# Performance work log

Hardware: AMD Instinct MI355X
Metric: run time of the kernel (lower is better)

Reference implementation:

```python
import jax, jax.numpy as jnp
import numpy as np

ROPE_BASE = 10000.0
WINDOW = 1024  # per_layer_sliding_window
SCALE = 0.08838834764831845  # 1/sqrt(128)
NEG_INF = -1e30


def _apply_rope(x, positions):
    # x: [B, S, H, D]; positions: [B, S] int
    D = x.shape[-1]
    inv_freq = 1.0 / (ROPE_BASE ** (jnp.arange(0, D, 2, dtype=jnp.float32) / D))  # [D/2]
    ang = positions.astype(jnp.float32)[..., None] * inv_freq          # [B, S, D/2]
    cos = jnp.cos(ang)[:, :, None, :]                                   # [B, S, 1, D/2]
    sin = jnp.sin(ang)[:, :, None, :]
    x1, x2 = x[..., : D // 2], x[..., D // 2 :]
    return jnp.concatenate([x1 * cos - x2 * sin, x2 * cos + x1 * sin], axis=-1)


def setup_inputs() -> dict:
    key = jax.random.key(0)
    k1, k2, k3, k4 = jax.random.split(key, 4)
    B, S, H, KV, D = 1, 2048, 32, 8, 128
    q = jax.random.normal(k1, (B, S, H, D), dtype=jnp.float32)
    k = jax.random.normal(k2, (B, S, KV, D), dtype=jnp.float32)
    v = jax.random.normal(k3, (B, S, KV, D), dtype=jnp.float32)
    positions = jnp.broadcast_to(jnp.arange(S, dtype=jnp.int32), (B, S))
    sinks = jax.random.normal(k4, (H,), dtype=jnp.float32)
    return {"q": q, "k": k, "v": v, "positions": positions, "sinks": sinks}


def reference(q, k, v, positions, sinks):
    # q: [B,S,H,D]; k,v: [B,S,KV,D]; positions: [B,S]; sinks: [H]
    B, S, H, D = q.shape
    KV = k.shape[2]
    group = H // KV

    qr = _apply_rope(q, positions)
    kr = _apply_rope(k, positions)

    # GQA: expand kv heads to match q heads
    kr = jnp.repeat(kr, group, axis=2)  # [B,S,H,D]
    ve = jnp.repeat(v, group, axis=2)   # [B,S,H,D]

    scores = jnp.einsum("bqhd,bkhd->bhqk", qr, kr) * SCALE  # [B,H,Q,K]

    pq = positions[:, :, None]  # [B,Q,1]
    pk = positions[:, None, :]  # [B,1,K]
    allowed = (pk <= pq) & (pq - pk < WINDOW)               # causal + sliding window
    scores = jnp.where(allowed[:, None, :, :], scores, NEG_INF)

    # softmax with per-head attention sink logit in the denominator
    sink = sinks[None, :, None]                             # [1,H,1]
    m = jnp.maximum(jnp.max(scores, axis=-1), sink)         # [B,H,Q]
    p = jnp.exp(scores - m[..., None])                      # [B,H,Q,K]
    denom = jnp.sum(p, axis=-1) + jnp.exp(sink - m)         # [B,H,Q]
    out = jnp.einsum("bhqk,bkhd->bqhd", p, ve) / denom.transpose(0, 2, 1)[..., None]
    return out  # [B,S,H,D]
```

## Files before the change

kernel.cpp:

```cpp
#include <hip/hip_runtime.h>

#define S_LEN 2048
#define NH 32
#define NKV 8
#define HD 128
#define WINDOW 1024
#define SCALEF 0.08838834764831845f
#define NEG_INF_F -1e30f
#define NEG_L2_10K_O64 -0.2076205059304601f
#define LOG2E 1.442695040888963f
#define CSHIFT_L2 17.31234049067355f

typedef unsigned short ushort_t;
typedef __attribute__((ext_vector_type(8))) short short8;
typedef __attribute__((ext_vector_type(4))) float floatx4;
typedef __attribute__((ext_vector_type(4))) int intx4;

static __device__ __forceinline__ float fexp2(float x) {
  return __builtin_amdgcn_exp2f(x);
}

static __device__ __forceinline__ ushort_t f2bf(float f) {
  union { float f; unsigned u; } un; un.f = f;
  unsigned r = un.u + 0x7fffu + ((un.u >> 16) & 1u);
  return (ushort_t)(r >> 16);
}

static __device__ __forceinline__ unsigned pack2bf(float a, float b) {
  return (unsigned)f2bf(a) | ((unsigned)f2bf(b) << 16);
}

__device__ __forceinline__ void gl_lds16(const ushort_t* g, ushort_t* l) {
  __builtin_amdgcn_global_load_lds(
      (const __attribute__((address_space(1))) unsigned int*)g,
      (__attribute__((address_space(3))) unsigned int*)l, 16, 0, 0);
}

__global__ __launch_bounds__(256) void prep_kv(
    const float* __restrict__ k, const float* __restrict__ v,
    const int* __restrict__ positions, ushort_t* __restrict__ Kr,
    ushort_t* __restrict__ Vt) {
  __shared__ float lv[64][129];
  const int kv = blockIdx.x & 7;
  const int s0 = (blockIdx.x >> 3) * 64;
  const int tid = threadIdx.x;

  {
    const int i = tid & 63;
    const int wrow = tid >> 6;
    const float invf = fexp2((float)i * NEG_L2_10K_O64);
#pragma unroll 4
    for (int it = 0; it < 16; ++it) {
      int s = s0 + it * 4 + wrow;
      float pos = (float)positions[s];
      const float* kp = k + ((size_t)s * NKV + kv) * HD;
      float x1 = kp[i], x2 = kp[i + 64];
      float sn, cs;
      __sincosf(pos * invf, &sn, &cs);
      ushort_t* o = Kr + ((size_t)kv * S_LEN + s) * HD;
      o[i] = f2bf(x1 * cs - x2 * sn);
      o[i + 64] = f2bf(x2 * cs + x1 * sn);
    }
  }
  {
    const int d = tid & 127;
    const int r2 = tid >> 7;
#pragma unroll
    for (int it = 0; it < 32; ++it) {
      int row = it * 2 + r2;
      lv[row][d] = v[((size_t)(s0 + row) * NKV + kv) * HD + d];
    }
  }
  __syncthreads();
  {
    const int ss = tid & 63;
    const int d0 = tid >> 6;
#pragma unroll
    for (int it = 0; it < 32; ++it) {
      int d = d0 + it * 4;
      Vt[((size_t)kv * HD + d) * S_LEN + s0 + ss] = f2bf(lv[ss][d]);
    }
  }
}

__global__ __launch_bounds__(256, 4) void attn_kernel(
    const float* __restrict__ q, const int* __restrict__ positions,
    const float* __restrict__ sinks, const ushort_t* __restrict__ Kr,
    const ushort_t* __restrict__ Vt, float* __restrict__ out) {
  __shared__ __align__(16) ushort_t smem[16384];

  const int tid = threadIdx.x;
  const int w = tid >> 6;
  const int lane = tid & 63;
  const int quad = lane >> 4;
  const int l16 = lane & 15;
  const int kv = blockIdx.x & 7;
  const int tile = blockIdx.x >> 3;
  const int h = kv * 4 + w;
  const int q0 = tile * 16;

  ushort_t* Qsw = smem + w * 2048;
  {
    const float invf = fexp2((float)lane * NEG_L2_10K_O64);
#pragma unroll 4
    for (int row = 0; row < 16; ++row) {
      float pos = (float)positions[q0 + row];
      const float* qp = q + ((size_t)(q0 + row) * NH + h) * HD;
      float x1 = qp[lane], x2 = qp[lane + 64];
      float sn, cs;
      __sincosf(pos * invf, &sn, &cs);
      float o1 = (x1 * cs - x2 * sn) * SCALEF;
      float o2 = (x2 * cs + x1 * sn) * SCALEF;
      int c1_ = (lane >> 3) ^ row;
      int c2_ = ((lane >> 3) + 8) ^ row;
      Qsw[row * 128 + c1_ * 8 + (lane & 7)] = f2bf(o1);
      Qsw[row * 128 + c2_ * 8 + (lane & 7)] = f2bf(o2);
    }
  }
  short8 qf[4];
#pragma unroll
  for (int t = 0; t < 4; ++t)
    qf[t] = *(const short8*)&Qsw[l16 * 128 + (((4 * t + quad) ^ l16) * 8)];
  __syncthreads();

  const ushort_t* KrH = Kr + (size_t)kv * S_LEN * HD;
  const ushort_t* VtH = Vt + (size_t)kv * HD * S_LEN;
  int kgo[2], vgo[2], ldst[2];
#pragma unroll
  for (int i = 0; i < 2; ++i) {
    int slot = i * 256 + tid;
    int key = slot >> 4;
    int cin = (slot & 15) ^ (key & 15);
    kgo[i] = key * HD + cin * 8;
    int d = slot >> 2;
    int qcin = (slot & 3) ^ ((d ^ (d >> 2)) & 3);
    vgo[i] = d * S_LEN + qcin * 8;
    ldst[i] = (i * 256 + (tid & 192)) * 8;
  }

  auto stage = [&](int b, int koff) {
#pragma unroll
    for (int i = 0; i < 2; ++i) {
      gl_lds16(KrH + (size_t)koff * HD + kgo[i], smem + b * 4096 + ldst[i]);
      gl_lds16(VtH + koff + vgo[i], smem + 8192 + b * 4096 + ldst[i]);
    }
  };

  floatx4 O4[8];
#pragma unroll
  for (int i = 0; i < 8; ++i) O4[i] = (floatx4){0.f, 0.f, 0.f, 0.f};
  float lsum = 0.f;

  const int cbeg = (q0 > 1023) ? ((q0 - 1023) >> 5) : 0;
  const int cend = (q0 + 15) >> 5;

  stage(0, cbeg * 32);
  __syncthreads();

  for (int ci = cbeg; ci <= cend; ++ci) {
    const int b = (ci - cbeg) & 1;
    const int koff = ci * 32;
    if (ci < cend) stage(b ^ 1, koff + 32);

    const ushort_t* KsB = smem + b * 4096;
    const ushort_t* VsB = smem + 8192 + b * 4096;

    floatx4 s0v = (floatx4){0.f, 0.f, 0.f, 0.f};
    floatx4 s1v = (floatx4){0.f, 0.f, 0.f, 0.f};
#pragma unroll
    for (int t = 0; t < 4; ++t) {
      int ch = ((4 * t + quad) ^ l16) * 8;
      short8 k0 = *(const short8*)&KsB[l16 * 128 + ch];
      short8 k1 = *(const short8*)&KsB[(l16 + 16) * 128 + ch];
      s0v = __builtin_amdgcn_mfma_f32_16x16x32_bf16(k0, qf[t], s0v, 0, 0, 0);
      s1v = __builtin_amdgcn_mfma_f32_16x16x32_bf16(k1, qf[t], s1v, 0, 0, 0);
    }

    if (koff + 31 > q0 || koff < q0 - 1008) {
      const int qp_ = q0 + l16;
#pragma unroll
      for (int r = 0; r < 4; ++r) {
        int k0i = koff + quad * 4 + r, k1i = k0i + 16;
        if (!((k0i <= qp_) && (qp_ - k0i < WINDOW))) s0v[r] = NEG_INF_F;
        if (!((k1i <= qp_) && (qp_ - k1i < WINDOW))) s1v[r] = NEG_INF_F;
      }
    }

    float pc0[4], pc1[4];
#pragma unroll
    for (int r = 0; r < 4; ++r) {
      pc0[r] = fexp2(fmaf(s0v[r], LOG2E, -CSHIFT_L2));
      pc1[r] = fexp2(fmaf(s1v[r], LOG2E, -CSHIFT_L2));
    }
    lsum += (pc0[0] + pc0[1]) + (pc0[2] + pc0[3]) +
            (pc1[0] + pc1[1]) + (pc1[2] + pc1[3]);

    unsigned pk0[2] = {pack2bf(pc0[0], pc0[1]), pack2bf(pc0[2], pc0[3])};
    unsigned pk1[2] = {pack2bf(pc1[0], pc1[1]), pack2bf(pc1[2], pc1[3])};
    intx4 bi;
    const int sbase = ((quad & 1) * 2) * 16 + l16;
#pragma unroll
    for (int u = 0; u < 4; ++u) {
      int src = sbase + (u >> 1) * 16;
      int lo = __shfl((int)pk0[u & 1], src);
      int hi = __shfl((int)pk1[u & 1], src);
      bi[u] = (quad < 2) ? lo : hi;
    }
    short8 pb = __builtin_bit_cast(short8, bi);

#pragma unroll
    for (int i = 0; i < 8; ++i) {
      int d = 16 * i + l16;
      short8 vf = *(const short8*)&VsB[d * 32 + ((quad ^ ((d ^ (d >> 2)) & 3)) * 8)];
      O4[i] = __builtin_amdgcn_mfma_f32_16x16x32_bf16(vf, pb, O4[i], 0, 0, 0);
    }

    __syncthreads();
  }

  lsum += __shfl_xor(lsum, 16);
  lsum += __shfl_xor(lsum, 32);
  lsum += fexp2(fmaf(sinks[h], LOG2E, -CSHIFT_L2));
  const float rl = 1.0f / lsum;

  float* op = out + ((size_t)(q0 + l16) * NH + h) * HD;
#pragma unroll
  for (int i = 0; i < 8; ++i) {
    floatx4 val = O4[i] * rl;
    *(floatx4*)(op + 16 * i + quad * 4) = val;
  }
}

extern "C" void kernel_launch(void* const* d_in, const int* in_sizes, int n_in,
                              void* d_out, int out_size, void* d_ws, size_t ws_size,
                              hipStream_t stream) {
  const float* q = (const float*)d_in[0];
  const float* k = (const float*)d_in[1];
  const float* v = (const float*)d_in[2];
  const int* positions = (const int*)d_in[3];
  const float* sinks = (const float*)d_in[4];
  float* out = (float*)d_out;

  ushort_t* Kr = (ushort_t*)d_ws;
  ushort_t* Vt = Kr + (size_t)NKV * S_LEN * HD;

  prep_kv<<<NKV * (S_LEN / 64), 256, 0, stream>>>(k, v, positions, Kr, Vt);
  attn_kernel<<<NKV * (S_LEN / 16), 256, 0, stream>>>(q, positions, sinks, Kr, Vt, out);
}
```

Before: 148.5 us.

## Restructure attention with 32x32 MFMA, key-split warps, paired tiles, and blocked V layout

Each warp now covers two query heads and half of each 32-key chunk, and uses 32x32x16 MFMAs for the PV product. Partial outputs from the two key halves are reduced through LDS at the end. Query tiles are paired (a short tile with a long one) so that 768 blocks carry balanced causal/window work. V is stored in 64-key blocked tiles, the softmax scale is folded into Q, and bf16 packing of probabilities uses a cheaper truncate-with-round-add plus perm. This adds LDS reduction traffic, more syncs, and fewer blocks with launch bounds lowered to 3.

```diff
diff --git a/kernel.cpp b/kernel.cpp
--- a/kernel.cpp
+++ b/kernel.cpp
@@ -5,15 +5,14 @@
 #define NKV 8
 #define HD 128
 #define WINDOW 1024
-#define SCALEF 0.08838834764831845f
 #define NEG_INF_F -1e30f
 #define NEG_L2_10K_O64 -0.2076205059304601f
-#define LOG2E 1.442695040888963f
-#define CSHIFT_L2 17.31234049067355f
+#define LOG2E_F 1.442695040888963f
 
 typedef unsigned short ushort_t;
 typedef __attribute__((ext_vector_type(8))) short short8;
 typedef __attribute__((ext_vector_type(4))) float floatx4;
+typedef __attribute__((ext_vector_type(16))) float floatx16;
 typedef __attribute__((ext_vector_type(4))) int intx4;
 
 static __device__ __forceinline__ float fexp2(float x) {
@@ -28,6 +27,12 @@
 
 static __device__ __forceinline__ unsigned pack2bf(float a, float b) {
   return (unsigned)f2bf(a) | ((unsigned)f2bf(b) << 16);
+}
+
+static __device__ __forceinline__ unsigned packP(float a, float b) {
+  unsigned ua = __builtin_bit_cast(unsigned, a) + 0x8000u;
+  unsigned ub = __builtin_bit_cast(unsigned, b) + 0x8000u;
+  return __builtin_amdgcn_perm(ub, ua, 0x07060302u);
 }
 
 __device__ __forceinline__ void gl_lds16(const ushort_t* g, ushort_t* l) {
@@ -44,7 +49,6 @@
   const int kv = blockIdx.x & 7;
   const int s0 = (blockIdx.x >> 3) * 64;
   const int tid = threadIdx.x;
-
   {
     const int i = tid & 63;
     const int wrow = tid >> 6;
@@ -73,161 +77,230 @@
   }
   __syncthreads();
   {
-    const int ss = tid & 63;
-    const int d0 = tid >> 6;
-#pragma unroll
-    for (int it = 0; it < 32; ++it) {
-      int d = d0 + it * 4;
-      Vt[((size_t)kv * HD + d) * S_LEN + s0 + ss] = f2bf(lv[ss][d]);
+    unsigned* Vreg = (unsigned*)(Vt + ((size_t)(kv * 32 + (s0 >> 6)) * HD) * 64);
+#pragma unroll
+    for (int it = 0; it < 16; ++it) {
+      int idx = it * 256 + tid;
+      int d = idx >> 5, j = idx & 31;
+      Vreg[idx] = pack2bf(lv[2 * j][d], lv[2 * j + 1][d]);
     }
   }
 }
 
-__global__ __launch_bounds__(256, 4) void attn_kernel(
+__global__ __launch_bounds__(256, 3) void attn_kernel(
     const float* __restrict__ q, const int* __restrict__ positions,
     const float* __restrict__ sinks, const ushort_t* __restrict__ Kr,
     const ushort_t* __restrict__ Vt, float* __restrict__ out) {
   __shared__ __align__(16) ushort_t smem[16384];
+  __shared__ float lsx[64];
 
   const int tid = threadIdx.x;
   const int w = tid >> 6;
   const int lane = tid & 63;
   const int quad = lane >> 4;
   const int l16 = lane & 15;
+  const int hp = w >> 1;
+  const int kh = w & 1;
   const int kv = blockIdx.x & 7;
-  const int tile = blockIdx.x >> 3;
-  const int h = kv * 4 + w;
-  const int q0 = tile * 16;
-
-  ushort_t* Qsw = smem + w * 2048;
-  {
-    const float invf = fexp2((float)lane * NEG_L2_10K_O64);
+  const int bid = blockIdx.x >> 3;
+  const int h0 = kv * 4 + hp * 2;
+  const float QSCALE = (float)(0.08838834764831845 * 1.4426950408889634);
+
+  const ushort_t* KrH = Kr + (size_t)kv * S_LEN * HD;
+  const ushort_t* VtH = Vt + (size_t)kv * 32 * HD * 64;
+
+  int tiles[2];
+  int ntiles;
+  if (bid < 64) { tiles[0] = bid + 64; tiles[1] = 0; ntiles = 1; }
+  else          { tiles[0] = bid - 64; tiles[1] = 127 - bid; ntiles = 2; }
+
+  int kgo0, kgo1, vgo0, vgo1;
+  { int key = tid >> 4;          kgo0 = key * HD + (((tid & 15) ^ (key & 15)) * 8); }
+  { int s2 = 256 + tid; int key = s2 >> 4;
+                                 kgo1 = key * HD + (((s2 & 15) ^ (key & 15)) * 8); }
+  { int d = tid >> 2;            vgo0 = d * 64 + (((tid & 3) ^ (d & 3)) * 8); }
+  { int d = 64 + (tid >> 2);     vgo1 = d * 64 + (((tid & 3) ^ (d & 3)) * 8); }
+  const int kdst0 = (tid & 192) * 8;
+  const int kdst1 = (256 + (tid & 192)) * 8;
+  const int vdst0 = 8192 + (tid & 192) * 8;
+  const int vdst1 = 8192 + 2048 + (tid & 192) * 8;
+  const int vroff = ((2 * kh + (lane >> 5)) ^ (lane & 3)) * 8;
+
+  auto stage = [&](int b, int koff) {
+    const ushort_t* kb = KrH + (size_t)koff * HD;
+    const ushort_t* vb = VtH + (size_t)(koff >> 6) * HD * 64 + (koff & 32);
+    gl_lds16(kb + kgo0, smem + b * 4096 + kdst0);
+    gl_lds16(kb + kgo1, smem + b * 4096 + kdst1);
+    gl_lds16(vb + vgo0, smem + b * 4096 + vdst0);
+    gl_lds16(vb + vgo1, smem + b * 4096 + vdst1);
+  };
+
+  for (int ti = 0; ti < ntiles; ++ti) {
+    const int tile = tiles[ti];
+    const int q0 = tile * 16;
+
+    {
+      const int hw = kv * 4 + w;
+      ushort_t* Qsw = smem + w * 2048;
+      const float invf = fexp2((float)lane * NEG_L2_10K_O64);
 #pragma unroll 4
-    for (int row = 0; row < 16; ++row) {
-      float pos = (float)positions[q0 + row];
-      const float* qp = q + ((size_t)(q0 + row) * NH + h) * HD;
-      float x1 = qp[lane], x2 = qp[lane + 64];
-      float sn, cs;
-      __sincosf(pos * invf, &sn, &cs);
-      float o1 = (x1 * cs - x2 * sn) * SCALEF;
-      float o2 = (x2 * cs + x1 * sn) * SCALEF;
-      int c1_ = (lane >> 3) ^ row;
-      int c2_ = ((lane >> 3) + 8) ^ row;
-      Qsw[row * 128 + c1_ * 8 + (lane & 7)] = f2bf(o1);
-      Qsw[row * 128 + c2_ * 8 + (lane & 7)] = f2bf(o2);
-    }
-  }
-  short8 qf[4];
-#pragma unroll
-  for (int t = 0; t < 4; ++t)
-    qf[t] = *(const short8*)&Qsw[l16 * 128 + (((4 * t + quad) ^ l16) * 8)];
-  __syncthreads();
-
-  const ushort_t* KrH = Kr + (size_t)kv * S_LEN * HD;
-  const ushort_t* VtH = Vt + (size_t)kv * HD * S_LEN;
-  int kgo[2], vgo[2], ldst[2];
-#pragma unroll
-  for (int i = 0; i < 2; ++i) {
-    int slot = i * 256 + tid;
-    int key = slot >> 4;
-    int cin = (slot & 15) ^ (key & 15);
-    kgo[i] = key * HD + cin * 8;
-    int d = slot >> 2;
-    int qcin = (slot & 3) ^ ((d ^ (d >> 2)) & 3);
-    vgo[i] = d * S_LEN + qcin * 8;
-    ldst[i] = (i * 256 + (tid & 192)) * 8;
-  }
-
-  auto stage = [&](int b, int koff) {
-#pragma unroll
-    for (int i = 0; i < 2; ++i) {
-      gl_lds16(KrH + (size_t)koff * HD + kgo[i], smem + b * 4096 + ldst[i]);
-      gl_lds16(VtH + koff + vgo[i], smem + 8192 + b * 4096 + ldst[i]);
-    }
-  };
-
-  floatx4 O4[8];
-#pragma unroll
-  for (int i = 0; i < 8; ++i) O4[i] = (floatx4){0.f, 0.f, 0.f, 0.f};
-  float lsum = 0.f;
-
-  const int cbeg = (q0 > 1023) ? ((q0 - 1023) >> 5) : 0;
-  const int cend = (q0 + 15) >> 5;
-
-  stage(0, cbeg * 32);
-  __syncthreads();
-
-  for (int ci = cbeg; ci <= cend; ++ci) {
-    const int b = (ci - cbeg) & 1;
-    const int koff = ci * 32;
-    if (ci < cend) stage(b ^ 1, koff + 32);
-
-    const ushort_t* KsB = smem + b * 4096;
-    const ushort_t* VsB = smem + 8192 + b * 4096;
-
-    floatx4 s0v = (floatx4){0.f, 0.f, 0.f, 0.f};
-    floatx4 s1v = (floatx4){0.f, 0.f, 0.f, 0.f};
-#pragma unroll
-    for (int t = 0; t < 4; ++t) {
-      int ch = ((4 * t + quad) ^ l16) * 8;
-      short8 k0 = *(const short8*)&KsB[l16 * 128 + ch];
-      short8 k1 = *(const short8*)&KsB[(l16 + 16) * 128 + ch];
-      s0v = __builtin_amdgcn_mfma_f32_16x16x32_bf16(k0, qf[t], s0v, 0, 0, 0);
-      s1v = __builtin_amdgcn_mfma_f32_16x16x32_bf16(k1, qf[t], s1v, 0, 0, 0);
-    }
-
-    if (koff + 31 > q0 || koff < q0 - 1008) {
-      const int qp_ = q0 + l16;
-#pragma unroll
-      for (int r = 0; r < 4; ++r) {
-        int k0i = koff + quad * 4 + r, k1i = k0i + 16;
-        if (!((k0i <= qp_) && (qp_ - k0i < WINDOW))) s0v[r] = NEG_INF_F;
-        if (!((k1i <= qp_) && (qp_ - k1i < WINDOW))) s1v[r] = NEG_INF_F;
-      }
-    }
-
-    float pc0[4], pc1[4];
-#pragma unroll
-    for (int r = 0; r < 4; ++r) {
-      pc0[r] = fexp2(fmaf(s0v[r], LOG2E, -CSHIFT_L2));
-      pc1[r] = fexp2(fmaf(s1v[r], LOG2E, -CSHIFT_L2));
-    }
-    lsum += (pc0[0] + pc0[1]) + (pc0[2] + pc0[3]) +
-            (pc1[0] + pc1[1]) + (pc1[2] + pc1[3]);
-
-    unsigned pk0[2] = {pack2bf(pc0[0], pc0[1]), pack2bf(pc0[2], pc0[3])};
-    unsigned pk1[2] = {pack2bf(pc1[0], pc1[1]), pack2bf(pc1[2], pc1[3])};
-    intx4 bi;
-    const int sbase = ((quad & 1) * 2) * 16 + l16;
-#pragma unroll
-    for (int u = 0; u < 4; ++u) {
-      int src = sbase + (u >> 1) * 16;
-      int lo = __shfl((int)pk0[u & 1], src);
-      int hi = __shfl((int)pk1[u & 1], src);
-      bi[u] = (quad < 2) ? lo : hi;
-    }
-    short8 pb = __builtin_bit_cast(short8, bi);
-
-#pragma unroll
-    for (int i = 0; i < 8; ++i) {
-      int d = 16 * i + l16;
-      short8 vf = *(const short8*)&VsB[d * 32 + ((quad ^ ((d ^ (d >> 2)) & 3)) * 8)];
-      O4[i] = __builtin_amdgcn_mfma_f32_16x16x32_bf16(vf, pb, O4[i], 0, 0, 0);
-    }
-
-    __syncthreads();
-  }
-
-  lsum += __shfl_xor(lsum, 16);
-  lsum += __shfl_xor(lsum, 32);
-  lsum += fexp2(fmaf(sinks[h], LOG2E, -CSHIFT_L2));
-  const float rl = 1.0f / lsum;
-
-  float* op = out + ((size_t)(q0 + l16) * NH + h) * HD;
-#pragma unroll
-  for (int i = 0; i < 8; ++i) {
-    floatx4 val = O4[i] * rl;
-    *(floatx4*)(op + 16 * i + quad * 4) = val;
+      for (int row = 0; row < 16; ++row) {
+        float pos = (float)positions[q0 + row];
+        const float* qp = q + ((size_t)(q0 + row) * NH + hw) * HD;
+        float x1 = qp[lane], x2 = qp[lane + 64];
+        float sn, cs;
+        __sincosf(pos * invf, &sn, &cs);
+        float o1 = (x1 * cs - x2 * sn) * QSCALE;
+        float o2 = (x2 * cs + x1 * sn) * QSCALE;
+        int c1_ = (lane >> 3) ^ row;
+        int c2_ = ((lane >> 3) + 8) ^ row;
+        Qsw[row * 128 + c1_ * 8 + (lane & 7)] = f2bf(o1);
+        Qsw[row * 128 + c2_ * 8 + (lane & 7)] = f2bf(o2);
+      }
+    }
+    __syncthreads();
+    short8 qf0[4], qf1[4];
+    {
+      const ushort_t* Qr0 = smem + (hp * 2) * 2048;
+      const ushort_t* Qr1 = smem + (hp * 2 + 1) * 2048;
+#pragma unroll
+      for (int t = 0; t < 4; ++t) {
+        int off = l16 * 128 + (((4 * t + quad) ^ l16) * 8);
+        qf0[t] = *(const short8*)&Qr0[off];
+        qf1[t] = *(const short8*)&Qr1[off];
+      }
+    }
+    __syncthreads();
+
+    floatx16 O[4];
+#pragma unroll
+    for (int i = 0; i < 4; ++i)
+#pragma unroll
+      for (int e = 0; e < 16; ++e) O[i][e] = 0.f;
+    float lsumA = 0.f, lsumB = 0.f;
+
+    const int cbeg = (q0 > 1023) ? ((q0 - 1023) >> 5) : 0;
+    const int cend = (q0 + 15) >> 5;
+
+    stage(0, cbeg * 32);
+    __syncthreads();
+
+    for (int ci = cbeg; ci <= cend; ++ci) {
+      const int b = (ci - cbeg) & 1;
+      const int koff = ci * 32;
+      if (ci < cend) stage(b ^ 1, koff + 32);
+
+      const ushort_t* KsB = smem + b * 4096 + (kh * 16) * 128;
+      floatx4 sA = {0.f, 0.f, 0.f, 0.f}, sB = {0.f, 0.f, 0.f, 0.f};
+#pragma unroll
+      for (int t = 0; t < 4; ++t) {
+        short8 kf = *(const short8*)&KsB[l16 * 128 + (((4 * t + quad) ^ l16) * 8)];
+        sA = __builtin_amdgcn_mfma_f32_16x16x32_bf16(kf, qf0[t], sA, 0, 0, 0);
+        sB = __builtin_amdgcn_mfma_f32_16x16x32_bf16(kf, qf1[t], sB, 0, 0, 0);
+      }
+
+      if (koff + 31 > q0 || koff < q0 - 1008) {
+        const int qp_ = q0 + l16;
+        const int kb_ = koff + kh * 16 + quad * 4;
+#pragma unroll
+        for (int r = 0; r < 4; ++r) {
+          int ki = kb_ + r;
+          bool ok = (ki <= qp_) && (qp_ - ki < WINDOW);
+          if (!ok) { sA[r] = NEG_INF_F; sB[r] = NEG_INF_F; }
+        }
+      }
+
+      float pA[4], pB[4];
+#pragma unroll
+      for (int r = 0; r < 4; ++r) { pA[r] = fexp2(sA[r]); pB[r] = fexp2(sB[r]); }
+      lsumA += (pA[0] + pA[1]) + (pA[2] + pA[3]);
+      lsumB += (pB[0] + pB[1]) + (pB[2] + pB[3]);
+
+      unsigned a01 = packP(pA[0], pA[1]), a23 = packP(pA[2], pA[3]);
+      unsigned b01 = packP(pB[0], pB[1]), b23 = packP(pB[2], pB[3]);
+      intx4 bi;
+      {
+        const int s0l = (quad >> 1) * 32 + l16;
+        int xa0 = __shfl((int)a01, s0l),      xa1 = __shfl((int)a23, s0l);
+        int xa2 = __shfl((int)a01, s0l + 16), xa3 = __shfl((int)a23, s0l + 16);
+        int yb0 = __shfl((int)b01, s0l),      yb1 = __shfl((int)b23, s0l);
+        int yb2 = __shfl((int)b01, s0l + 16), yb3 = __shfl((int)b23, s0l + 16);
+        const bool hb = (quad & 1);
+        bi[0] = hb ? yb0 : xa0; bi[1] = hb ? yb1 : xa1;
+        bi[2] = hb ? yb2 : xa2; bi[3] = hb ? yb3 : xa3;
+      }
+      short8 pf = __builtin_bit_cast(short8, bi);
+
+      const ushort_t* VsB = smem + 8192 + b * 4096;
+#pragma unroll
+      for (int tl = 0; tl < 4; ++tl) {
+        short8 vf = *(const short8*)&VsB[(tl * 32 + (lane & 31)) * 32 + vroff];
+        O[tl] = __builtin_amdgcn_mfma_f32_32x32x16_bf16(vf, pf, O[tl], 0, 0, 0);
+      }
+
+      __syncthreads();
+    }
+
+    lsumA += __shfl_xor(lsumA, 16); lsumA += __shfl_xor(lsumA, 32);
+    lsumB += __shfl_xor(lsumB, 16); lsumB += __shfl_xor(lsumB, 32);
+    float* Lf = (float*)smem;
+    const int lfb = hp * 2560 + lane * 20;
+    float rl = 0.f;
+
+    if (kh == 1) {
+      if (quad == 0) {
+        lsx[hp * 32 + l16] = lsumA;
+        lsx[hp * 32 + 16 + l16] = lsumB;
+      }
+#pragma unroll
+      for (int u = 0; u < 2; ++u)
+#pragma unroll
+        for (int r4 = 0; r4 < 4; ++r4)
+          *(floatx4*)&Lf[lfb + u * 1280 + r4 * 4] =
+              (floatx4){O[u][r4 * 4], O[u][r4 * 4 + 1], O[u][r4 * 4 + 2], O[u][r4 * 4 + 3]};
+    }
+    __syncthreads();
+    if (kh == 0) {
+      float denA = lsumA + lsx[hp * 32 + l16] + fexp2(sinks[h0] * LOG2E_F);
+      float denB = lsumB + lsx[hp * 32 + 16 + l16] + fexp2(sinks[h0 + 1] * LOG2E_F);
+      rl = (quad & 1) ? (1.0f / denB) : (1.0f / denA);
+      float* op = out + ((size_t)(q0 + l16) * NH + (h0 + (quad & 1))) * HD;
+#pragma unroll
+      for (int u = 0; u < 2; ++u)
+#pragma unroll
+        for (int r4 = 0; r4 < 4; ++r4) {
+          floatx4 pv = *(const floatx4*)&Lf[lfb + u * 1280 + r4 * 4];
+          floatx4 vv;
+#pragma unroll
+          for (int e = 0; e < 4; ++e) vv[e] = (O[u][r4 * 4 + e] + pv[e]) * rl;
+          *(floatx4*)(op + u * 32 + r4 * 8 + (quad >> 1) * 4) = vv;
+        }
+    }
+    __syncthreads();
+    if (kh == 1) {
+#pragma unroll
+      for (int u = 0; u < 2; ++u)
+#pragma unroll
+        for (int r4 = 0; r4 < 4; ++r4)
+          *(floatx4*)&Lf[lfb + u * 1280 + r4 * 4] =
+              (floatx4){O[u + 2][r4 * 4], O[u + 2][r4 * 4 + 1],
+                        O[u + 2][r4 * 4 + 2], O[u + 2][r4 * 4 + 3]};
+    }
+    __syncthreads();
+    if (kh == 0) {
+      float* op = out + ((size_t)(q0 + l16) * NH + (h0 + (quad & 1))) * HD;
+#pragma unroll
+      for (int u = 0; u < 2; ++u)
+#pragma unroll
+        for (int r4 = 0; r4 < 4; ++r4) {
+          floatx4 pv = *(const floatx4*)&Lf[lfb + u * 1280 + r4 * 4];
+          floatx4 vv;
+#pragma unroll
+          for (int e = 0; e < 4; ++e) vv[e] = (O[u + 2][r4 * 4 + e] + pv[e]) * rl;
+          *(floatx4*)(op + (u + 2) * 32 + r4 * 8 + (quad >> 1) * 4) = vv;
+        }
+    }
+    __syncthreads();
   }
 }
 
@@ -245,5 +318,5 @@
   ushort_t* Vt = Kr + (size_t)NKV * S_LEN * HD;
 
   prep_kv<<<NKV * (S_LEN / 64), 256, 0, stream>>>(k, v, positions, Kr, Vt);
-  attn_kernel<<<NKV * (S_LEN / 16), 256, 0, stream>>>(q, positions, sinks, Kr, Vt, out);
-}
+  attn_kernel<<<NKV * 96, 256, 0, stream>>>(q, positions, sinks, Kr, Vt, out);
+}
```

After: 143.6 us. -3.3%, faster.
